# Kernel optimization log

Measured on AMD Instinct MI355X. Metric: run time of the kernel, lower is better.

Reference implementation:

```python
import jax, jax.numpy as jnp
import numpy as np

B, T, ENC, DEC, U = 64, 2048, 512, 512, 128

def setup_inputs() -> dict:
    key = jax.random.key(0)
    ks = jax.random.split(key, 8)
    s_dec = 1.0 / np.sqrt(DEC)
    s_enc = 1.0 / np.sqrt(ENC)
    s_u = 1.0 / np.sqrt(U)
    return {
        "decoder_hidden": jax.random.normal(ks[0], (B, DEC), jnp.float32),
        "encoder_outputs": jax.random.normal(ks[1], (B, T, ENC), jnp.float32),
        "Wa": jax.random.normal(ks[2], (DEC, U), jnp.float32) * s_dec,
        "ba": jnp.zeros((U,), jnp.float32),
        "Wb": jax.random.normal(ks[3], (ENC, U), jnp.float32) * s_enc,
        "bb": jnp.zeros((U,), jnp.float32),
        "Wv": jax.random.normal(ks[4], (U, 1), jnp.float32) * s_u,
        "bv": jnp.zeros((1,), jnp.float32),
    }

def reference(decoder_hidden, encoder_outputs, Wa, ba, Wb, bb, Wv, bv):
    # q: [B, 1, U] — decoder hidden projected, broadcast over time
    q = (decoder_hidden @ Wa + ba)[:, None, :]
    # k: [B, T, U]
    k = jnp.einsum('bte,eu->btu', encoder_outputs, Wb) + bb
    # score: [B, T, 1]
    score = jnp.tanh(q + k) @ Wv + bv
    attn = jax.nn.softmax(score, axis=1)          # [B, T, 1]
    context = jnp.sum(attn * encoder_outputs, axis=1)  # [B, ENC]
    return context, attn
```

## Files before the change

kernel.cpp:

```cpp
#include <hip/hip_runtime.h>
#include <math.h>

#define B_   64
#define T_   2048
#define ENC_ 512
#define U_   128
#define NC   16
#define MBLK 128

typedef __attribute__((ext_vector_type(8))) _Float16 half8;
typedef __attribute__((ext_vector_type(4))) float float4v;

__device__ __forceinline__ void async_ld16(const void* g, void* l) {
    __builtin_amdgcn_global_load_lds(
        (const __attribute__((address_space(1))) void*)g,
        (__attribute__((address_space(3))) void*)l, 16, 0, 0);
}

__device__ inline void cvt_split8_f16(const float4 a0, const float4 a1,
                                      half8& h, half8& l) {
    const float xs[8] = {a0.x, a0.y, a0.z, a0.w, a1.x, a1.y, a1.z, a1.w};
#pragma unroll
    for (int j = 0; j < 8; ++j) {
        const _Float16 hi = (_Float16)xs[j];
        h[j] = hi;
        l[j] = (_Float16)(xs[j] - (float)hi);
    }
}

__device__ inline float fast_tanh(float x) {
    const float e = __expf(2.0f * x);
    return 1.0f - 2.0f / (e + 1.0f);
}

__global__ __launch_bounds__(256)
void prep_kernel(const float* __restrict__ dh,
                 const float* __restrict__ Wa,
                 const float* __restrict__ ba,
                 const float* __restrict__ bb,
                 const float* __restrict__ Wb,
                 float* __restrict__ q,
                 _Float16* __restrict__ whf,
                 float* __restrict__ uz) {
    const int blk = blockIdx.x;
    const int tid = threadIdx.x;
    if (blk < 64) {
        if (tid < U_) {
            const int b = blk, u = tid;
            const float* dhb = dh + b * ENC_;
            float a0 = 0.f, a1 = 0.f, a2 = 0.f, a3 = 0.f;
#pragma unroll 4
            for (int e = 0; e < ENC_; e += 4) {
                a0 += dhb[e + 0] * Wa[(e + 0) * U_ + u];
                a1 += dhb[e + 1] * Wa[(e + 1) * U_ + u];
                a2 += dhb[e + 2] * Wa[(e + 2) * U_ + u];
                a3 += dhb[e + 3] * Wa[(e + 3) * U_ + u];
            }
            q[b * U_ + u] = ((a0 + a1) + (a2 + a3)) + ba[u] + bb[u];
        }
    } else if (blk < 96) {
        const int fid = (blk - 64) * 4 + (tid >> 6);
        const int c   = fid >> 3;
        const int gn  = fid & 7;
        const int L   = tid & 63;
        const int n   = gn * 16 + (L & 15);
        const int k0  = c * 32 + (L >> 4) * 8;
        half8 hi;
#pragma unroll
        for (int j = 0; j < 8; ++j)
            hi[j] = (_Float16)Wb[(size_t)(k0 + j) * U_ + n];
        *(half8*)(whf + ((size_t)fid * 64 + L) * 8) = hi;
    } else {
        const int i = (blk - 96) * 256 + tid;
        if (i < B_ * ENC_ + B_) uz[i] = 0.f;
    }
}

__global__ __launch_bounds__(256, 3)
void score_ctx_kernel(const float* __restrict__ enc,
                      const _Float16* __restrict__ whf,
                      const float* __restrict__ q,
                      const float* __restrict__ Wv,
                      float* __restrict__ expw,
                      float* __restrict__ uctx,
                      float* __restrict__ Zsum) {
    __shared__ __align__(16) float    As[2][4096];
    __shared__ __align__(16) _Float16 Bs[2][4096];
    __shared__ float ew[MBLK];

    const int tid = threadIdx.x;
    const int w   = tid >> 6;
    const int L   = tid & 63;
    const int m0  = blockIdx.x * MBLK;
    const int b   = m0 >> 11;

    const int arow = w * 32 + (L >> 3);
    const int akf  = ((L & 7) ^ (L >> 3)) * 4;
    const float* aprow = enc + (size_t)(m0 + arow) * ENC_ + akf;
    const _Float16* bprow = whf + w * 1024 + L * 8;

    float4v acc[2][8];
#pragma unroll
    for (int mi = 0; mi < 2; ++mi)
#pragma unroll
        for (int gi = 0; gi < 8; ++gi) acc[mi][gi] = (float4v)0.f;

    {
#pragma unroll
        for (int j = 0; j < 4; ++j)
            async_ld16(aprow + (size_t)j * 8 * ENC_, &As[0][w * 1024 + j * 256]);
#pragma unroll
        for (int j = 0; j < 2; ++j)
            async_ld16(bprow + j * 512, &Bs[0][w * 1024 + j * 512]);
    }
    __syncthreads();

    for (int c = 0; c < NC; ++c) {
        const int cur = c & 1;

        if (c < NC - 1) {
            const int nxt = cur ^ 1;
            const float* ap = aprow + (c + 1) * 32;
#pragma unroll
            for (int j = 0; j < 4; ++j)
                async_ld16(ap + (size_t)j * 8 * ENC_, &As[nxt][w * 1024 + j * 256]);
            const _Float16* bp = bprow + (size_t)(c + 1) * 4096;
#pragma unroll
            for (int j = 0; j < 2; ++j)
                async_ld16(bp + j * 512, &Bs[nxt][w * 1024 + j * 512]);
        }

        half8 bh[8];
#pragma unroll
        for (int gi = 0; gi < 8; ++gi)
            bh[gi] = *(const half8*)(&Bs[cur][(gi * 64 + L) * 8]);

        half8 ah[2], al[2];
#pragma unroll
        for (int mi = 0; mi < 2; ++mi) {
            const int row = w * 32 + mi * 16 + (L & 15);
            const int s4  = (row & 7) * 4;
            const int k0  = (L >> 4) * 8;
            const float4 x0 = *(const float4*)(&As[cur][row * 32 + (k0 ^ s4)]);
            const float4 x1 = *(const float4*)(&As[cur][row * 32 + ((k0 + 4) ^ s4)]);
            cvt_split8_f16(x0, x1, ah[mi], al[mi]);
        }

#pragma unroll
        for (int mi = 0; mi < 2; ++mi)
#pragma unroll
            for (int gi = 0; gi < 8; ++gi) {
                acc[mi][gi] = __builtin_amdgcn_mfma_f32_16x16x32_f16(ah[mi], bh[gi], acc[mi][gi], 0, 0, 0);
                acc[mi][gi] = __builtin_amdgcn_mfma_f32_16x16x32_f16(al[mi], bh[gi], acc[mi][gi], 0, 0, 0);
            }

        __syncthreads();
    }

    const int n15 = L & 15;
    float qv[8], wvv[8];
#pragma unroll
    for (int gi = 0; gi < 8; ++gi) {
        const int u = gi * 16 + n15;
        qv[gi]  = q[b * U_ + u];
        wvv[gi] = Wv[u];
    }
#pragma unroll
    for (int mi = 0; mi < 2; ++mi) {
#pragma unroll
        for (int r = 0; r < 4; ++r) {
            float s = 0.f;
#pragma unroll
            for (int gi = 0; gi < 8; ++gi)
                s += fast_tanh(qv[gi] + acc[mi][gi][r]) * wvv[gi];
            s += __shfl_xor(s, 1, 64);
            s += __shfl_xor(s, 2, 64);
            s += __shfl_xor(s, 4, 64);
            s += __shfl_xor(s, 8, 64);
            if (n15 == 0) {
                const int mrow = w * 32 + mi * 16 + (L >> 4) * 4 + r;
                const float e = __expf(s);
                ew[mrow] = e;
                expw[m0 + mrow] = e;
            }
        }
    }
    __syncthreads();

    const int col = tid * 2;
    const float* ebase = enc + (size_t)m0 * ENC_ + col;
    float sx = 0.f, sy = 0.f;
#pragma unroll 8
    for (int t = 0; t < MBLK; ++t) {
        const float wgt = ew[t];
        const float2 v = *(const float2*)(ebase + (size_t)t * ENC_);
        sx += wgt * v.x;
        sy += wgt * v.y;
    }
    atomicAdd(&uctx[b * ENC_ + col], sx);
    atomicAdd(&uctx[b * ENC_ + col + 1], sy);

    if (tid < 64) {
        float z = ew[tid] + ew[tid + 64];
        z += __shfl_xor(z, 1, 64);
        z += __shfl_xor(z, 2, 64);
        z += __shfl_xor(z, 4, 64);
        z += __shfl_xor(z, 8, 64);
        z += __shfl_xor(z, 16, 64);
        z += __shfl_xor(z, 32, 64);
        if (tid == 0) atomicAdd(&Zsum[b], z);
    }
}

__global__ void normalize_kernel(const float* __restrict__ uctx,
                                 const float* __restrict__ Zsum,
                                 const float* __restrict__ expw,
                                 float* __restrict__ ctx,
                                 float* __restrict__ attn) {
    const int idx = blockIdx.x * 256 + threadIdx.x;
    if (idx < B_ * ENC_) {
        ctx[idx] = uctx[idx] / Zsum[idx >> 9];
    } else {
        const int i2 = idx - B_ * ENC_;
        attn[i2] = expw[i2] / Zsum[i2 >> 11];
    }
}

extern "C" void kernel_launch(void* const* d_in, const int* in_sizes, int n_in,
                              void* d_out, int out_size, void* d_ws, size_t ws_size,
                              hipStream_t stream) {
    const float* dh  = (const float*)d_in[0];
    const float* enc = (const float*)d_in[1];
    const float* Wa  = (const float*)d_in[2];
    const float* ba  = (const float*)d_in[3];
    const float* Wb  = (const float*)d_in[4];
    const float* bb  = (const float*)d_in[5];
    const float* Wv  = (const float*)d_in[6];

    float* out      = (float*)d_out;
    float* ctx      = out;
    float* attn_out = out + (B_ * ENC_);

    float* ws   = (float*)d_ws;
    float* q    = ws;
    float* expw = ws + 8192;
    float* uctx = ws + 8192 + B_ * T_;
    float* Zs   = uctx + B_ * ENC_;
    _Float16* whf = (_Float16*)(Zs + 64);

    prep_kernel<<<225, 256, 0, stream>>>(dh, Wa, ba, bb, Wb, q, whf, uctx);
    score_ctx_kernel<<<(B_ * T_) / MBLK, 256, 0, stream>>>(enc, whf, q, Wv,
                                                           expw, uctx, Zs);
    normalize_kernel<<<(B_ * (ENC_ + T_)) / 256, 256, 0, stream>>>(uctx, Zs, expw,
                                                                   ctx, attn_out);
}
```

Baseline: 437.8 us.

## Load encoder tiles straight to registers, drop LDS staging, halve block rows

After: 480.5 us. +9.7%, slower.

```diff
diff --git a/kernel.cpp b/kernel.cpp
--- a/kernel.cpp
+++ b/kernel.cpp
@@ -6,16 +6,10 @@
 #define ENC_ 512
 #define U_   128
 #define NC   16
-#define MBLK 128
+#define MBLK 64
 
 typedef __attribute__((ext_vector_type(8))) _Float16 half8;
 typedef __attribute__((ext_vector_type(4))) float float4v;
-
-__device__ __forceinline__ void async_ld16(const void* g, void* l) {
-    __builtin_amdgcn_global_load_lds(
-        (const __attribute__((address_space(1))) void*)g,
-        (__attribute__((address_space(3))) void*)l, 16, 0, 0);
-}
 
 __device__ inline void cvt_split8_f16(const float4 a0, const float4 a1,
                                       half8& h, half8& l) {
@@ -84,80 +78,54 @@
                       float* __restrict__ expw,
                       float* __restrict__ uctx,
                       float* __restrict__ Zsum) {
-    __shared__ __align__(16) float    As[2][4096];
-    __shared__ __align__(16) _Float16 Bs[2][4096];
     __shared__ float ew[MBLK];
 
     const int tid = threadIdx.x;
     const int w   = tid >> 6;
     const int L   = tid & 63;
-    const int m0  = blockIdx.x * MBLK;
+    const int wg  = ((blockIdx.x & 7) << 8) | (blockIdx.x >> 3);
+    const int m0  = wg * MBLK;
     const int b   = m0 >> 11;
 
-    const int arow = w * 32 + (L >> 3);
-    const int akf  = ((L & 7) ^ (L >> 3)) * 4;
-    const float* aprow = enc + (size_t)(m0 + arow) * ENC_ + akf;
-    const _Float16* bprow = whf + w * 1024 + L * 8;
-
-    float4v acc[2][8];
-#pragma unroll
-    for (int mi = 0; mi < 2; ++mi)
-#pragma unroll
-        for (int gi = 0; gi < 8; ++gi) acc[mi][gi] = (float4v)0.f;
-
-    {
-#pragma unroll
-        for (int j = 0; j < 4; ++j)
-            async_ld16(aprow + (size_t)j * 8 * ENC_, &As[0][w * 1024 + j * 256]);
-#pragma unroll
-        for (int j = 0; j < 2; ++j)
-            async_ld16(bprow + j * 512, &Bs[0][w * 1024 + j * 512]);
-    }
-    __syncthreads();
-
-    for (int c = 0; c < NC; ++c) {
-        const int cur = c & 1;
-
-        if (c < NC - 1) {
-            const int nxt = cur ^ 1;
-            const float* ap = aprow + (c + 1) * 32;
-#pragma unroll
-            for (int j = 0; j < 4; ++j)
-                async_ld16(ap + (size_t)j * 8 * ENC_, &As[nxt][w * 1024 + j * 256]);
-            const _Float16* bp = bprow + (size_t)(c + 1) * 4096;
-#pragma unroll
-            for (int j = 0; j < 2; ++j)
-                async_ld16(bp + j * 512, &Bs[nxt][w * 1024 + j * 512]);
-        }
-
-        half8 bh[8];
-#pragma unroll
-        for (int gi = 0; gi < 8; ++gi)
-            bh[gi] = *(const half8*)(&Bs[cur][(gi * 64 + L) * 8]);
-
-        half8 ah[2], al[2];
-#pragma unroll
-        for (int mi = 0; mi < 2; ++mi) {
-            const int row = w * 32 + mi * 16 + (L & 15);
-            const int s4  = (row & 7) * 4;
-            const int k0  = (L >> 4) * 8;
-            const float4 x0 = *(const float4*)(&As[cur][row * 32 + (k0 ^ s4)]);
-            const float4 x1 = *(const float4*)(&As[cur][row * 32 + ((k0 + 4) ^ s4)]);
-            cvt_split8_f16(x0, x1, ah[mi], al[mi]);
-        }
-
-#pragma unroll
-        for (int mi = 0; mi < 2; ++mi)
+    const int n15 = L & 15;
+    const int aq  = L >> 4;
+    const float* aprow = enc + (size_t)(m0 + w * 16 + n15) * ENC_ + aq * 8;
+
+    float4v acc[8];
+#pragma unroll
+    for (int gi = 0; gi < 8; ++gi) acc[gi] = (float4v)0.f;
+
+    float4 xs[2][8];
+#pragma unroll
+    for (int j = 0; j < 8; ++j)
+        xs[0][j] = *(const float4*)(aprow + (j >> 1) * 32 + (j & 1) * 4);
+
+#pragma unroll
+    for (int sc = 0; sc < 4; ++sc) {
+        const int cur = sc & 1, nxt = cur ^ 1;
+        if (sc < 3) {
+#pragma unroll
+            for (int j = 0; j < 8; ++j)
+                xs[nxt][j] = *(const float4*)(aprow + (sc + 1) * 128 +
+                                              (j >> 1) * 32 + (j & 1) * 4);
+        }
+#pragma unroll
+        for (int c = 0; c < 4; ++c) {
+            const int cc = sc * 4 + c;
+            half8 bh[8];
+#pragma unroll
+            for (int gi = 0; gi < 8; ++gi)
+                bh[gi] = *(const half8*)(whf + ((size_t)(cc * 8 + gi) * 64 + L) * 8);
+            half8 ah, al;
+            cvt_split8_f16(xs[cur][2 * c], xs[cur][2 * c + 1], ah, al);
 #pragma unroll
             for (int gi = 0; gi < 8; ++gi) {
-                acc[mi][gi] = __builtin_amdgcn_mfma_f32_16x16x32_f16(ah[mi], bh[gi], acc[mi][gi], 0, 0, 0);
-                acc[mi][gi] = __builtin_amdgcn_mfma_f32_16x16x32_f16(al[mi], bh[gi], acc[mi][gi], 0, 0, 0);
+                acc[gi] = __builtin_amdgcn_mfma_f32_16x16x32_f16(ah, bh[gi], acc[gi], 0, 0, 0);
+                acc[gi] = __builtin_amdgcn_mfma_f32_16x16x32_f16(al, bh[gi], acc[gi], 0, 0, 0);
             }
-
-        __syncthreads();
-    }
-
-    const int n15 = L & 15;
+        }
+    }
+
     float qv[8], wvv[8];
 #pragma unroll
     for (int gi = 0; gi < 8; ++gi) {
@@ -166,23 +134,20 @@
         wvv[gi] = Wv[u];
     }
 #pragma unroll
-    for (int mi = 0; mi < 2; ++mi) {
-#pragma unroll
-        for (int r = 0; r < 4; ++r) {
-            float s = 0.f;
-#pragma unroll
-            for (int gi = 0; gi < 8; ++gi)
-                s += fast_tanh(qv[gi] + acc[mi][gi][r]) * wvv[gi];
-            s += __shfl_xor(s, 1, 64);
-            s += __shfl_xor(s, 2, 64);
-            s += __shfl_xor(s, 4, 64);
-            s += __shfl_xor(s, 8, 64);
-            if (n15 == 0) {
-                const int mrow = w * 32 + mi * 16 + (L >> 4) * 4 + r;
-                const float e = __expf(s);
-                ew[mrow] = e;
-                expw[m0 + mrow] = e;
-            }
+    for (int r = 0; r < 4; ++r) {
+        float s = 0.f;
+#pragma unroll
+        for (int gi = 0; gi < 8; ++gi)
+            s += fast_tanh(qv[gi] + acc[gi][r]) * wvv[gi];
+        s += __shfl_xor(s, 1, 64);
+        s += __shfl_xor(s, 2, 64);
+        s += __shfl_xor(s, 4, 64);
+        s += __shfl_xor(s, 8, 64);
+        if (n15 == 0) {
+            const int row = w * 16 + aq * 4 + r;
+            const float e = __expf(s);
+            ew[row] = e;
+            expw[m0 + row] = e;
         }
     }
     __syncthreads();
@@ -200,8 +165,8 @@
     atomicAdd(&uctx[b * ENC_ + col], sx);
     atomicAdd(&uctx[b * ENC_ + col + 1], sy);
 
-    if (tid < 64) {
-        float z = ew[tid] + ew[tid + 64];
+    if (tid < MBLK) {
+        float z = ew[tid];
         z += __shfl_xor(z, 1, 64);
         z += __shfl_xor(z, 2, 64);
         z += __shfl_xor(z, 4, 64);
```
